# Performance work log

Measured on AMD Instinct MI355X. Metric: run time of the kernel, lower is better.

Reference implementation:

```python
import jax, jax.numpy as jnp
import numpy as np

B, S, D, C, H, E, K, L = 32, 512, 768, 3072, 1024, 8, 2, 2


def _layernorm(x, g, b, eps=1e-5):
    mu = jnp.mean(x, axis=-1, keepdims=True)
    var = jnp.var(x, axis=-1, keepdims=True)
    return (x - mu) * jax.lax.rsqrt(var + eps) * g + b


def setup_inputs() -> dict:
    key = jax.random.key(0)
    ks = jax.random.split(key, 12)
    s = 0.02
    return {
        "hidden_states": jax.random.normal(ks[0], (B, S, C), jnp.float32),
        "proj_w": jax.random.normal(ks[1], (C, D), jnp.float32) * s,
        "proj_b": jnp.zeros((D,), jnp.float32),
        "ln1_g": jnp.ones((D,), jnp.float32),
        "ln1_b": jnp.zeros((D,), jnp.float32),
        "gate_w": jax.random.normal(ks[2], (D, E), jnp.float32) * s,
        "gate_b": jnp.zeros((E,), jnp.float32),
        "w1": jax.random.normal(ks[3], (E, D, H), jnp.float32) * s,
        "b1": jnp.zeros((E, H), jnp.float32),
        "w2": jax.random.normal(ks[4], (E, H, D), jnp.float32) * s,
        "b2": jnp.zeros((E, D), jnp.float32),
        "ln2_g": jnp.ones((D,), jnp.float32),
        "ln2_b": jnp.zeros((D,), jnp.float32),
        "cls_w": jax.random.normal(ks[5], (D, L), jnp.float32) * s,
        "cls_b": jnp.zeros((L,), jnp.float32),
    }


def reference(hidden_states, proj_w, proj_b, ln1_g, ln1_b, gate_w, gate_b,
              w1, b1, w2, b2, ln2_g, ln2_b, cls_w, cls_b):
    # layer_projection: Linear -> LayerNorm -> GELU (dropout = identity in eval)
    x = jnp.einsum('bsc,cd->bsd', hidden_states, proj_w) + proj_b
    x = _layernorm(x, ln1_g, ln1_b)
    seq_out = jax.nn.gelu(x, approximate=False)  # [B,S,D]

    # Router: gate -> softmax -> top-k -> renormalize
    probs = jax.nn.softmax(seq_out @ gate_w + gate_b, axis=-1)  # [B,S,E]
    top_w, top_i = jax.lax.top_k(probs, K)                      # [B,S,K]
    top_w = top_w / jnp.sum(top_w, axis=-1, keepdims=True)

    # combine[t,e] = sum_k top_w[t,k] * (top_i[t,k]==e)
    combine = jnp.sum(jax.nn.one_hot(top_i, E, dtype=top_w.dtype)
                      * top_w[..., None], axis=-2)              # [B,S,E]

    xt = seq_out.reshape(-1, D)                                 # [T,D]
    ct = combine.reshape(-1, E)                                 # [T,E]
    h = jax.nn.gelu(jnp.einsum('td,edh->eth', xt, w1) + b1[:, None, :],
                    approximate=False)                          # [E,T,H]
    eo = jnp.einsum('eth,ehd->etd', h, w2) + b2[:, None, :]     # [E,T,D]
    moe = jnp.einsum('etd,te->td', eo, ct).reshape(B, S, D)

    moe = _layernorm(moe + seq_out, ln2_g, ln2_b)
    logits = moe @ cls_w + cls_b                                # [B,S,2]
    return logits
```

## Files before the change

kernel.cpp:

```cpp
#include <hip/hip_runtime.h>
#include <hip/hip_bf16.h>

#define T_TOK 16384
#define CDIM 3072
#define DDIM 768
#define HDIM 1024
#define NEXP 8
#define NSLOT 33792
#define MAXTILE 264
#define AMB_CAP 2048
#define AMB2_CAP 256
#define KSPLIT 4
#define NSEG 8

typedef __attribute__((ext_vector_type(8))) short bfrag;
typedef __attribute__((ext_vector_type(4))) float f32x4;
typedef __attribute__((ext_vector_type(4))) float fvec4;

__device__ __forceinline__ unsigned short bf16_rn(float f) {
  union { float f; unsigned u; } v; v.f = f;
  unsigned r = v.u + 0x7fffu + ((v.u >> 16) & 1u);
  return (unsigned short)(r >> 16);
}
__device__ __forceinline__ float bf16_f32(unsigned short h) {
  union { unsigned u; float f; } v; v.u = ((unsigned)h) << 16;
  return v.f;
}
__device__ __forceinline__ float gelu_exact(float x) {
  return 0.5f * x * (1.0f + erff(x * 0.70710678118654752440f));
}
__device__ __forceinline__ void glds16(const void* g, void* l) {
  __builtin_amdgcn_global_load_lds((const __attribute__((address_space(1))) void*)g,
                                   (__attribute__((address_space(3))) void*)l, 16, 0, 0);
}

__global__ void k_init(int* token_list, int* counts, int* cursors, unsigned short* zero_row,
                       int* amb_count, int* amb2_count) {
  int i = blockIdx.x * 256 + threadIdx.x;
  for (int j = i; j < NSLOT; j += 64 * 256) token_list[j] = -1;
  if (i < NEXP) counts[i] = 0;
  if (i < 128) cursors[i] = 0;
  if (i == 0) { *amb_count = 0; *amb2_count = 0; }
  if (i < 1024) zero_row[i] = 0;
}

__global__ void k_cast_tiled(const float* __restrict__ src,
                             unsigned short* __restrict__ dst) {
  __shared__ unsigned short h[128][136];
  int rb = blockIdx.x;
  int cc = blockIdx.y;
  int tid = threadIdx.x;
  const float* in = src + ((size_t)rb * 128) * CDIM + cc * 128;
#pragma unroll
  for (int it = 0; it < 16; ++it) {
    int idx = it * 256 + tid;
    int r = idx >> 5, nv = idx & 31;
    fvec4 v = *(const fvec4*)(in + (size_t)r * CDIM + nv * 4);
    unsigned long long p = (unsigned long long)bf16_rn(v[0]) |
                           ((unsigned long long)bf16_rn(v[1]) << 16) |
                           ((unsigned long long)bf16_rn(v[2]) << 32) |
                           ((unsigned long long)bf16_rn(v[3]) << 48);
    *(unsigned long long*)&h[r][nv * 4] = p;
  }
  __syncthreads();
  unsigned short* ob = dst + ((size_t)rb * 96 + cc * 4) * 4096;
#pragma unroll
  for (int kt = 0; kt < 4; ++kt) {
#pragma unroll
    for (int it = 0; it < 2; ++it) {
      int gg = it * 256 + tid;
      int kg = gg >> 7, r = gg & 127;
      bfrag o = *(const bfrag*)&h[r][kt * 32 + kg * 8];
      *(bfrag*)(ob + ((size_t)kt * 512 + gg) * 8) = o;
    }
  }
}

__global__ void k_transpose_split(const float* __restrict__ src,
                                  unsigned short* __restrict__ dhi,
                                  unsigned short* __restrict__ dlo) {
  __shared__ unsigned short h[128][72], l[128][72];
  int nb2 = blockIdx.x;
  int cb = blockIdx.y;
  int col_blk = nb2 >> 1, nhalf = nb2 & 1;
  int n0 = col_blk * 128 + nhalf * 64;
  int tid = threadIdx.x;
  const float* in = src + (size_t)(cb * 128) * DDIM + n0;
#pragma unroll
  for (int it = 0; it < 8; ++it) {
    int idx = it * 256 + tid;
    int cl = idx >> 4, nv = idx & 15;
    fvec4 v = *(const fvec4*)(in + (size_t)cl * DDIM + nv * 4);
    unsigned long long ph = 0, pl = 0;
#pragma unroll
    for (int e = 0; e < 4; ++e) {
      unsigned short hh = bf16_rn(v[e]);
      unsigned short ll = bf16_rn(v[e] - bf16_f32(hh));
      ph |= (unsigned long long)hh << (16 * e);
      pl |= (unsigned long long)ll << (16 * e);
    }
    *(unsigned long long*)&h[cl][nv * 4] = ph;
    *(unsigned long long*)&l[cl][nv * 4] = pl;
  }
  __syncthreads();
  size_t obase = ((size_t)col_blk * 96 + cb * 4) * 4096;
#pragma unroll
  for (int kt = 0; kt < 4; ++kt) {
    int kg = tid >> 6, rl = tid & 63;
    bfrag oh, ol;
#pragma unroll
    for (int e = 0; e < 8; ++e) {
      int c = kt * 32 + kg * 8 + e;
      oh[e] = (short)h[c][rl];
      ol[e] = (short)l[c][rl];
    }
    size_t gi = obase + ((size_t)kt * 512 + kg * 128 + nhalf * 64 + rl) * 8;
    *(bfrag*)(dhi + gi) = oh;
    *(bfrag*)(dlo + gi) = ol;
  }
}

__global__ void k_transpose_tiled(const float* __restrict__ src0,
                                  unsigned short* __restrict__ dst0, int K, int N) {
  __shared__ unsigned short h[128][72];
  int nb2 = blockIdx.x;
  int cb = blockIdx.y;
  int z = blockIdx.z;
  int col_blk = nb2 >> 1, nhalf = nb2 & 1;
  int n0 = col_blk * 128 + nhalf * 64;
  int tid = threadIdx.x;
  const float* in = src0 + (size_t)z * K * N + (size_t)(cb * 128) * N + n0;
#pragma unroll
  for (int it = 0; it < 8; ++it) {
    int idx = it * 256 + tid;
    int cl = idx >> 4, nv = idx & 15;
    fvec4 v = *(const fvec4*)(in + (size_t)cl * N + nv * 4);
    unsigned long long ph = 0;
#pragma unroll
    for (int e = 0; e < 4; ++e)
      ph |= (unsigned long long)bf16_rn(v[e]) << (16 * e);
    *(unsigned long long*)&h[cl][nv * 4] = ph;
  }
  __syncthreads();
  size_t obase = (size_t)z * K * N + ((size_t)col_blk * (K / 32) + cb * 4) * 4096;
#pragma unroll
  for (int kt = 0; kt < 4; ++kt) {
    int kg = tid >> 6, rl = tid & 63;
    bfrag oh;
#pragma unroll
    for (int e = 0; e < 8; ++e) oh[e] = (short)h[kt * 32 + kg * 8 + e][rl];
    *(bfrag*)(dst0 + obase + ((size_t)kt * 512 + kg * 128 + nhalf * 64 + rl) * 8) = oh;
  }
}

__launch_bounds__(256, 3)
__global__ void k_gemm1(const unsigned short* __restrict__ Atil,
                        const unsigned short* __restrict__ Btil,
                        float* __restrict__ Cout)
{
  __shared__ unsigned short sA[12288], sB[12288];
  int tid = threadIdx.x;
  int lane = tid & 63, wave = tid >> 6;
  int id = blockIdx.x;
  int swz = (id & 7) * 96 + (id >> 3);
  int brow = swz / 6, bcol = swz % 6;
  int row0 = brow * 128, col0 = bcol * 128;
  int wm = wave >> 1, wn = wave & 1;

  f32x4 acc[4][4];
#pragma unroll
  for (int i = 0; i < 4; ++i)
#pragma unroll
    for (int j = 0; j < 4; ++j) acc[i][j] = (f32x4){0.f, 0.f, 0.f, 0.f};

  int rsel = lane & 15, kq = lane >> 4;
  const unsigned short* At = Atil + (size_t)(brow * 96) * 4096;
  const unsigned short* Bt = Btil + (size_t)(bcol * 96) * 4096;

  auto STAGE = [&](int kt, int b) {
    const unsigned short* as = At + (size_t)kt * 4096;
    const unsigned short* bs = Bt + (size_t)kt * 4096;
    int lbase = b * 4096;
#pragma unroll
    for (int pass = 0; pass < 2; ++pass) {
      int g = pass * 256 + tid;
      int li = lbase + (pass * 256 + wave * 64) * 8;
      glds16(as + (size_t)g * 8, &sA[li]);
      glds16(bs + (size_t)g * 8, &sB[li]);
    }
  };

  STAGE(0, 0);
  STAGE(1, 1);
  int b0 = 0;
  for (int kt = 0; kt < 96; ++kt) {
    if (kt < 95) asm volatile("s_waitcnt vmcnt(4)" ::: "memory");
    else         asm volatile("s_waitcnt vmcnt(0)" ::: "memory");
    __builtin_amdgcn_s_barrier();
    if (kt + 2 < 96) {
      int bn = b0 + 2; if (bn >= 3) bn -= 3;
      STAGE(kt + 2, bn);
    }
    int lb = b0 * 4096;
    bfrag af[4], bf[4];
#pragma unroll
    for (int i = 0; i < 4; ++i) {
      af[i] = *(const bfrag*)&sA[lb + (kq * 128 + wm * 64 + i * 16 + rsel) * 8];
      bf[i] = *(const bfrag*)&sB[lb + (kq * 128 + wn * 64 + i * 16 + rsel) * 8];
    }
#pragma unroll
    for (int i = 0; i < 4; ++i)
#pragma unroll
      for (int j = 0; j < 4; ++j)
        acc[i][j] = __builtin_amdgcn_mfma_f32_16x16x32_bf16(af[i], bf[j], acc[i][j], 0, 0, 0);
    b0 = (b0 == 2) ? 0 : b0 + 1;
  }

  int cc = lane & 15, rr = (lane >> 4) * 4;
#pragma unroll
  for (int i = 0; i < 4; ++i)
#pragma unroll
    for (int j = 0; j < 4; ++j)
#pragma unroll
      for (int r = 0; r < 4; ++r) {
        int row = row0 + wm * 64 + i * 16 + rr + r;
        int col = col0 + wn * 64 + j * 16 + cc;
        Cout[(size_t)row * DDIM + col] = acc[i][j][r];
      }
}

__launch_bounds__(256)
__global__ void k_ln_router(const float* __restrict__ xw, const float* __restrict__ proj_b,
                            const float* __restrict__ g1, const float* __restrict__ b1v,
                            const float* __restrict__ gate_w, const float* __restrict__ gate_b,
                            unsigned short* __restrict__ seq_b16,
                            int* __restrict__ top_i, float* __restrict__ top_w,
                            int* __restrict__ amb_list, int* __restrict__ amb_count)
{
  int lane = threadIdx.x & 63;
  int t = blockIdx.x * 4 + (threadIdx.x >> 6);
  const float* xr = xw + (size_t)t * DDIM;
  float x0[12];
  float s = 0.f, s2 = 0.f;
#pragma unroll
  for (int j = 0; j < 12; ++j) {
    int d = lane + 64 * j;
    float v = xr[d] + proj_b[d];
    x0[j] = v; s += v; s2 += v * v;
  }
#pragma unroll
  for (int o = 32; o > 0; o >>= 1) { s += __shfl_xor(s, o, 64); s2 += __shfl_xor(s2, o, 64); }
  float mu = s * (1.f / DDIM);
  float rstd = rsqrtf(s2 * (1.f / DDIM) - mu * mu + 1e-5f);
  float acc8[8];
#pragma unroll
  for (int e = 0; e < 8; ++e) acc8[e] = 0.f;
#pragma unroll
  for (int j = 0; j < 12; ++j) {
    int d = lane + 64 * j;
    float y = (x0[j] - mu) * rstd * g1[d] + b1v[d];
    float ge = gelu_exact(y);
    seq_b16[(size_t)t * DDIM + d] = bf16_rn(ge);
    const float* gw = gate_w + (size_t)d * NEXP;
#pragma unroll
    for (int e = 0; e < 8; ++e) acc8[e] += ge * gw[e];
  }
#pragma unroll
  for (int e = 0; e < 8; ++e)
#pragma unroll
    for (int o = 32; o > 0; o >>= 1) acc8[e] += __shfl_xor(acc8[e], o, 64);
  if (lane == 0) {
    float lg[8];
#pragma unroll
    for (int e = 0; e < 8; ++e) lg[e] = acc8[e] + gate_b[e];
    int i0 = 0;
    for (int e = 1; e < 8; ++e) if (lg[e] > lg[i0]) i0 = e;
    int i1 = (i0 == 0) ? 1 : 0;
    for (int e = 0; e < 8; ++e) if (e != i0 && lg[e] > lg[i1]) i1 = e;
    float l2 = -1e30f;
    for (int e = 0; e < 8; ++e) if (e != i0 && e != i1 && lg[e] > l2) l2 = lg[e];
    if (lg[i1] - l2 < 8e-3f) {
      int p = atomicAdd(amb_count, 1);
      if (p < AMB_CAP) amb_list[p] = t;
    }
    float w0 = 1.f / (1.f + expf(lg[i1] - lg[i0]));
    top_i[t * 2] = i0; top_i[t * 2 + 1] = i1;
    top_w[t * 2] = w0; top_w[t * 2 + 1] = 1.f - w0;
  }
}

__launch_bounds__(256, 2)
__global__ void k_repair(const float* __restrict__ hidden,
                         const unsigned short* __restrict__ BTh,
                         const unsigned short* __restrict__ BTl,
                         const int* __restrict__ amb_list, const int* __restrict__ amb_count,
                         float* __restrict__ xw_fix4)
{
  int n = *amb_count; if (n > AMB_CAP) n = AMB_CAP;
  int by = blockIdx.y;
  if (by * 128 >= n) return;
  int bx = blockIdx.x;
  int z = blockIdx.z;
  int col0 = bx * 128;
  __shared__ unsigned short sAh[8192], sAl[8192], sBh[8192], sBl[8192];
  __shared__ int tk[128];
  int tid = threadIdx.x, lane = tid & 63, wave = tid >> 6;
  if (tid < 128) tk[tid] = (by * 128 + tid < n) ? amb_list[by * 128 + tid] : -1;
  __syncthreads();
  int wm = wave >> 1, wn = wave & 1;
  f32x4 acc[4][4];
#pragma unroll
  for (int i = 0; i < 4; ++i)
#pragma unroll
    for (int j = 0; j < 4; ++j) acc[i][j] = (f32x4){0.f, 0.f, 0.f, 0.f};
  int rsel = lane & 15, kq = lane >> 4;
  int ktbase = z * 24;
  const unsigned short* Bth = BTh + (size_t)(bx * 96) * 4096;
  const unsigned short* Btl = BTl + (size_t)(bx * 96) * 4096;

  auto STAGE = [&](int kt, int b) {
    int k0 = (ktbase + kt) * 32;
    int lb = b * 4096;
    size_t tb = (size_t)(ktbase + kt) * 4096;
#pragma unroll
    for (int pass = 0; pass < 2; ++pass) {
      int g = pass * 256 + tid;
      int kg = g >> 7, r = g & 127;
      int tok = tk[r];
      fvec4 a0 = (fvec4){0.f, 0.f, 0.f, 0.f}, a1 = a0;
      if (tok >= 0) {
        const float* ap = hidden + (size_t)tok * CDIM + k0 + kg * 8;
        a0 = *(const fvec4*)ap;
        a1 = *(const fvec4*)(ap + 4);
      }
      bfrag hv, lv;
#pragma unroll
      for (int u = 0; u < 8; ++u) {
        float v = (u < 4) ? a0[u] : a1[u - 4];
        unsigned short h = bf16_rn(v);
        hv[u] = (short)h;
        lv[u] = (short)bf16_rn(v - bf16_f32(h));
      }
      *(bfrag*)&sAh[lb + (size_t)g * 8] = hv;
      *(bfrag*)&sAl[lb + (size_t)g * 8] = lv;
      int li = lb + (pass * 256 + wave * 64) * 8;
      glds16(Bth + tb + (size_t)g * 8, &sBh[li]);
      glds16(Btl + tb + (size_t)g * 8, &sBl[li]);
    }
  };

  STAGE(0, 0);
  __syncthreads();
  for (int kt = 0; kt < 24; ++kt) {
    int b = kt & 1;
    if (kt + 1 < 24) STAGE(kt + 1, b ^ 1);
    int lb = b * 4096;
    bfrag ah[4], al[4], bh[4], bl[4];
#pragma unroll
    for (int i = 0; i < 4; ++i) {
      int ra = wm * 64 + i * 16 + rsel;
      ah[i] = *(const bfrag*)&sAh[lb + (kq * 128 + ra) * 8];
      al[i] = *(const bfrag*)&sAl[lb + (kq * 128 + ra) * 8];
      int cb = wn * 64 + i * 16 + rsel;
      bh[i] = *(const bfrag*)&sBh[lb + (kq * 128 + cb) * 8];
      bl[i] = *(const bfrag*)&sBl[lb + (kq * 128 + cb) * 8];
    }
#pragma unroll
    for (int i = 0; i < 4; ++i)
#pragma unroll
      for (int j = 0; j < 4; ++j) {
        acc[i][j] = __builtin_amdgcn_mfma_f32_16x16x32_bf16(ah[i], bh[j], acc[i][j], 0, 0, 0);
        acc[i][j] = __builtin_amdgcn_mfma_f32_16x16x32_bf16(ah[i], bl[j], acc[i][j], 0, 0, 0);
        acc[i][j] = __builtin_amdgcn_mfma_f32_16x16x32_bf16(al[i], bh[j], acc[i][j], 0, 0, 0);
      }
    __syncthreads();
  }
  float* dst = xw_fix4 + (size_t)z * AMB_CAP * DDIM;
  int cc = lane & 15, rr = (lane >> 4) * 4;
#pragma unroll
  for (int i = 0; i < 4; ++i)
#pragma unroll
    for (int j = 0; j < 4; ++j)
#pragma unroll
      for (int r = 0; r < 4; ++r) {
        int row = by * 128 + wm * 64 + i * 16 + rr + r;
        int col = col0 + wn * 64 + j * 16 + cc;
        dst[(size_t)row * DDIM + col] = acc[i][j][r];
      }
}

__launch_bounds__(256)
__global__ void k_fix2(const float* __restrict__ xw_fix4, const float* __restrict__ proj_b,
                       const float* __restrict__ g1, const float* __restrict__ b1v,
                       const float* __restrict__ gate_w, const float* __restrict__ gate_b,
                       const int* __restrict__ amb_list, const int* __restrict__ amb_count,
                       int* __restrict__ top_i, float* __restrict__ top_w,
                       int* __restrict__ amb2_list, int* __restrict__ amb2_count)
{
  int n = *amb_count; if (n > AMB_CAP) n = AMB_CAP;
  int lane = threadIdx.x & 63;
  int slot = blockIdx.x * 4 + (threadIdx.x >> 6);
  if (slot >= n) return;
  int t = amb_list[slot];
  const float* p0 = xw_fix4 + (size_t)slot * DDIM;
  const float* p1 = p0 + (size_t)AMB_CAP * DDIM;
  const float* p2 = p1 + (size_t)AMB_CAP * DDIM;
  const float* p3 = p2 + (size_t)AMB_CAP * DDIM;
  float x0[12];
  float s = 0.f, s2 = 0.f;
#pragma unroll
  for (int j = 0; j < 12; ++j) {
    int d = lane + 64 * j;
    float v = ((p0[d] + p1[d]) + (p2[d] + p3[d])) + proj_b[d];
    x0[j] = v; s += v; s2 += v * v;
  }
#pragma unroll
  for (int o = 32; o > 0; o >>= 1) { s += __shfl_xor(s, o, 64); s2 += __shfl_xor(s2, o, 64); }
  float mu = s * (1.f / DDIM);
  float rstd = rsqrtf(s2 * (1.f / DDIM) - mu * mu + 1e-5f);
  float acc8[8];
#pragma unroll
  for (int e = 0; e < 8; ++e) acc8[e] = 0.f;
#pragma unroll
  for (int j = 0; j < 12; ++j) {
    int d = lane + 64 * j;
    float y = (x0[j] - mu) * rstd * g1[d] + b1v[d];
    float ge = gelu_exact(y);
    const float* gw = gate_w + (size_t)d * NEXP;
#pragma unroll
    for (int e = 0; e < 8; ++e) acc8[e] += ge * gw[e];
  }
#pragma unroll
  for (int e = 0; e < 8; ++e)
#pragma unroll
    for (int o = 32; o > 0; o >>= 1) acc8[e] += __shfl_xor(acc8[e], o, 64);
  if (lane == 0) {
    float lg[8];
#pragma unroll
    for (int e = 0; e < 8; ++e) lg[e] = acc8[e] + gate_b[e];
    int i0 = 0;
    for (int e = 1; e < 8; ++e) if (lg[e] > lg[i0]) i0 = e;
    int i1 = (i0 == 0) ? 1 : 0;
    for (int e = 0; e < 8; ++e) if (e != i0 && lg[e] > lg[i1]) i1 = e;
    float l2 = -1e30f;
    for (int e = 0; e < 8; ++e) if (e != i0 && e != i1 && lg[e] > l2) l2 = lg[e];
    if (lg[i1] - l2 < 2e-4f) {
      int p = atomicAdd(amb2_count, 1);
      if (p < AMB2_CAP) amb2_list[p] = t;
    }
    float w0 = 1.f / (1.f + expf(lg[i1] - lg[i0]));
    top_i[t * 2] = i0; top_i[t * 2 + 1] = i1;
    top_w[t * 2] = w0; top_w[t * 2 + 1] = 1.f - w0;
  }
}

__launch_bounds__(256, 1)
__global__ void k_router_fix(const float* __restrict__ hidden, const float* __restrict__ proj_w,
                             const int* __restrict__ amb2_list, const int* __restrict__ amb2_count,
                             double* __restrict__ xpart)
{
  __shared__ float hrow[384];
  int tid = threadIdx.x;
  int seg = blockIdx.y;
  int cbase = seg * 384;
  int n = *amb2_count; if (n > AMB2_CAP) n = AMB2_CAP;
  for (int ii = blockIdx.x; ii < n; ii += gridDim.x) {
    int t = amb2_list[ii];
    __syncthreads();
    if (tid < 96)
      *(fvec4*)&hrow[tid * 4] = *(const fvec4*)(hidden + (size_t)t * CDIM + cbase + tid * 4);
    __syncthreads();
    double p0a = 0.0, p0b = 0.0, p1a = 0.0, p1b = 0.0, p2a = 0.0, p2b = 0.0;
    for (int c0 = 0; c0 < 384; c0 += 16) {
      float w0r[16], w1r[16], w2r[16];
      const float* wp = proj_w + (size_t)(cbase + c0) * DDIM + tid;
#pragma unroll
      for (int u = 0; u < 16; ++u) {
        w0r[u] = wp[u * DDIM];
        w1r[u] = wp[u * DDIM + 256];
        w2r[u] = wp[u * DDIM + 512];
      }
#pragma unroll
      for (int u = 0; u < 16; ++u) {
        double h = (double)hrow[c0 + u];
        if (u & 1) { p0b += h * (double)w0r[u]; p1b += h * (double)w1r[u]; p2b += h * (double)w2r[u]; }
        else       { p0a += h * (double)w0r[u]; p1a += h * (double)w1r[u]; p2a += h * (double)w2r[u]; }
      }
    }
    double* xp = xpart + ((size_t)seg * AMB2_CAP + ii) * DDIM;
    xp[tid] = p0a + p0b;
    xp[tid + 256] = p1a + p1b;
    xp[tid + 512] = p2a + p2b;
  }
}

__launch_bounds__(256)
__global__ void k_fix3(const double* __restrict__ xpart, const float* __restrict__ proj_b,
                       const float* __restrict__ g1, const float* __restrict__ b1v,
                       const float* __restrict__ gate_w, const float* __restrict__ gate_b,
                       const int* __restrict__ amb2_list, const int* __restrict__ amb2_count,
                       int* __restrict__ top_i, float* __restrict__ top_w)
{
  __shared__ double redA[4], redB[4], red8[4][8];
  int n = *amb2_count; if (n > AMB2_CAP) n = AMB2_CAP;
  int ii = blockIdx.x;
  if (ii >= n) return;
  int t = amb2_list[ii];
  int tid = threadIdx.x, lane = tid & 63, wave = tid >> 6;
  double x[3]; double s = 0.0, s2 = 0.0;
#pragma unroll
  for (int j = 0; j < 3; ++j) {
    int d = tid + 256 * j;
    double acc = (double)proj_b[d];
#pragma unroll
    for (int seg = 0; seg < NSEG; ++seg)
      acc += xpart[((size_t)seg * AMB2_CAP + ii) * DDIM + d];
    x[j] = acc; s += acc; s2 += acc * acc;
  }
#pragma unroll
  for (int o = 32; o > 0; o >>= 1) { s += __shfl_down(s, o, 64); s2 += __shfl_down(s2, o, 64); }
  if (lane == 0) { redA[wave] = s; redB[wave] = s2; }
  __syncthreads();
  double mu = (redA[0] + redA[1] + redA[2] + redA[3]) / DDIM;
  double ms = (redB[0] + redB[1] + redB[2] + redB[3]) / DDIM;
  double rstd = 1.0 / sqrt(ms - mu * mu + 1e-5);
  double a8[8];
#pragma unroll
  for (int e = 0; e < 8; ++e) a8[e] = 0.0;
#pragma unroll
  for (int j = 0; j < 3; ++j) {
    int d = tid + 256 * j;
    double y = (x[j] - mu) * rstd * (double)g1[d] + (double)b1v[d];
    double ge = 0.5 * y * (1.0 + erf(y * 0.7071067811865475244));
#pragma unroll
    for (int e = 0; e < 8; ++e) a8[e] += ge * (double)gate_w[(size_t)d * NEXP + e];
  }
#pragma unroll
  for (int e = 0; e < 8; ++e)
#pragma unroll
    for (int o = 32; o > 0; o >>= 1) a8[e] += __shfl_down(a8[e], o, 64);
  if (lane == 0) {
#pragma unroll
    for (int e = 0; e < 8; ++e) red8[wave][e] = a8[e];
  }
  __syncthreads();
  if (tid == 0) {
    double lg[8];
#pragma unroll
    for (int e = 0; e < 8; ++e)
      lg[e] = red8[0][e] + red8[1][e] + red8[2][e] + red8[3][e] + (double)gate_b[e];
    int i0 = 0;
    for (int e = 1; e < 8; ++e) if (lg[e] > lg[i0]) i0 = e;
    int i1 = (i0 == 0) ? 1 : 0;
    for (int e = 0; e < 8; ++e) if (e != i0 && e != i1 && lg[e] > lg[i1]) i1 = e;
    double w0 = 1.0 / (1.0 + exp(lg[i1] - lg[i0]));
    top_i[t * 2] = i0; top_i[t * 2 + 1] = i1;
    top_w[t * 2] = (float)w0; top_w[t * 2 + 1] = (float)(1.0 - w0);
  }
}

__global__ void k_count(const int* __restrict__ top_i, int* __restrict__ counts) {
  __shared__ int h[NEXP];
  int tid = threadIdx.x;
  if (tid < NEXP) h[tid] = 0;
  __syncthreads();
  for (int i = blockIdx.x * 256 + tid; i < 2 * T_TOK; i += 64 * 256)
    atomicAdd(&h[top_i[i]], 1);
  __syncthreads();
  if (tid < NEXP) atomicAdd(&counts[tid], h[tid]);
}

__global__ void k_offsets(const int* __restrict__ counts, int* __restrict__ seg_start,
                          int* __restrict__ padded_total, int* __restrict__ tile_expert) {
  if (threadIdx.x != 0 || blockIdx.x != 0) return;
  int st[NEXP], en[NEXP];
  int s = 0;
  for (int e = 0; e < NEXP; ++e) {
    st[e] = s; seg_start[e] = s;
    s += (counts[e] + 127) & ~127;
    en[e] = s;
  }
  *padded_total = s;
  int nt = s >> 7;
  for (int x = 0; x < nt; ++x) {
    int r = x << 7, e = 0;
    for (int q = 0; q < NEXP; ++q) if (r >= st[q] && r < en[q]) e = q;
    tile_expert[x] = e;
  }
}

__global__ void k_scatter(const int* __restrict__ top_i, const int* __restrict__ seg_start,
                          int* __restrict__ cursors, int* __restrict__ token_list,
                          int* __restrict__ slot_of) {
  __shared__ int lc[NEXP];
  __shared__ int lbase[NEXP];
  int tid = threadIdx.x;
  int t = blockIdx.x * 256 + tid;
  if (tid < NEXP) lc[tid] = 0;
  __syncthreads();
  int e0 = top_i[t * 2], e1 = top_i[t * 2 + 1];
  int o0 = atomicAdd(&lc[e0], 1);
  int o1 = atomicAdd(&lc[e1], 1);
  __syncthreads();
  if (tid < NEXP) lbase[tid] = atomicAdd(&cursors[tid << 4], lc[tid]);
  __syncthreads();
  int p0 = seg_start[e0] + lbase[e0] + o0;
  int p1 = seg_start[e1] + lbase[e1] + o1;
  token_list[p0] = t;
  token_list[p1] = t;
  slot_of[t * 2] = p0;
  slot_of[t * 2 + 1] = p1;
}

__global__ void k_gather(const unsigned short* __restrict__ seqb,
                         const int* __restrict__ token_list,
                         const int* __restrict__ padded_total,
                         unsigned short* __restrict__ seqgT) {
  int sb = blockIdx.x;
  if (sb * 128 >= *padded_total) return;
  int cc = blockIdx.y;
  __shared__ unsigned short h[128][136];
  __shared__ int tk[128];
  int tid = threadIdx.x;
  if (tid < 128) tk[tid] = token_list[sb * 128 + tid];
  __syncthreads();
#pragma unroll
  for (int it = 0; it < 8; ++it) {
    int idx = it * 256 + tid;
    int r = idx >> 4, nv = idx & 15;
    int tok = tk[r];
    bfrag v = (bfrag){0, 0, 0, 0, 0, 0, 0, 0};
    if (tok >= 0)
      v = *(const bfrag*)(seqb + (size_t)tok * DDIM + cc * 128 + nv * 8);
    *(bfrag*)&h[r][nv * 8] = v;
  }
  __syncthreads();
  unsigned short* ob = seqgT + ((size_t)sb * 24 + cc * 4) * 4096;
#pragma unroll
  for (int kt = 0; kt < 4; ++kt) {
#pragma unroll
    for (int it = 0; it < 2; ++it) {
      int gg = it * 256 + tid;
      int kg = gg >> 7, r = gg & 127;
      bfrag o = *(const bfrag*)&h[r][kt * 32 + kg * 8];
      *(bfrag*)(ob + ((size_t)kt * 512 + gg) * 8) = o;
    }
  }
}

__launch_bounds__(256, 3)
__global__ void k_gemm2(const unsigned short* __restrict__ seqgT,
                        const unsigned short* __restrict__ w1T,
                        const float* __restrict__ b1,
                        const int* __restrict__ tile_expert,
                        const int* __restrict__ padded_total,
                        unsigned short* __restrict__ hbufT)
{
  int oid = blockIdx.x;
  int xcd = oid & 7, w = oid >> 3;
  int by = xcd * 33 + (w >> 3);
  int bx = w & 7;
  if (by * 128 >= *padded_total) return;
  int e = tile_expert[by];
  __shared__ unsigned short smem[24576];
  unsigned short* sA = smem;
  unsigned short* sB = smem + 12288;
  int tid = threadIdx.x, lane = tid & 63, wave = tid >> 6;
  int col0 = bx * 128;
  int wm = wave >> 1, wn = wave & 1;
  f32x4 acc[4][4];
#pragma unroll
  for (int i = 0; i < 4; ++i)
#pragma unroll
    for (int j = 0; j < 4; ++j) acc[i][j] = (f32x4){0.f, 0.f, 0.f, 0.f};
  const unsigned short* At = seqgT + (size_t)by * 24 * 4096;
  const unsigned short* Bt = w1T + (size_t)e * HDIM * DDIM + (size_t)bx * 24 * 4096;
  int rsel = lane & 15, kq = lane >> 4;

  auto STAGE = [&](int kt, int b) {
    int lbase2 = b * 4096;
    size_t tb = (size_t)kt * 4096;
#pragma unroll
    for (int pass = 0; pass < 2; ++pass) {
      int g = pass * 256 + tid;
      int li = lbase2 + (pass * 256 + wave * 64) * 8;
      glds16(At + tb + (size_t)g * 8, &sA[li]);
      glds16(Bt + tb + (size_t)g * 8, &sB[li]);
    }
  };

  STAGE(0, 0);
  STAGE(1, 1);
  int b0 = 0;
  for (int kt = 0; kt < 24; ++kt) {
    if (kt < 23) asm volatile("s_waitcnt vmcnt(4)" ::: "memory");
    else         asm volatile("s_waitcnt vmcnt(0)" ::: "memory");
    __builtin_amdgcn_s_barrier();
    if (kt + 2 < 24) {
      int bn = b0 + 2; if (bn >= 3) bn -= 3;
      STAGE(kt + 2, bn);
    }
    int lb = b0 * 4096;
    bfrag af[4], bf[4];
#pragma unroll
    for (int i = 0; i < 4; ++i) {
      af[i] = *(const bfrag*)&sA[lb + (kq * 128 + wm * 64 + i * 16 + rsel) * 8];
      bf[i] = *(const bfrag*)&sB[lb + (kq * 128 + wn * 64 + i * 16 + rsel) * 8];
    }
#pragma unroll
    for (int i = 0; i < 4; ++i)
#pragma unroll
      for (int j = 0; j < 4; ++j)
        acc[i][j] = __builtin_amdgcn_mfma_f32_16x16x32_bf16(af[i], bf[j], acc[i][j], 0, 0, 0);
    b0 = (b0 == 2) ? 0 : b0 + 1;
  }
  __builtin_amdgcn_s_barrier();
  int cc = lane & 15, rr = (lane >> 4) * 4;
#pragma unroll
  for (int i = 0; i < 4; ++i)
#pragma unroll
    for (int j = 0; j < 4; ++j)
#pragma unroll
      for (int r = 0; r < 4; ++r) {
        int lr = wm * 64 + i * 16 + rr + r;
        int lc = wn * 64 + j * 16 + cc;
        float x = acc[i][j][r] + b1[(size_t)e * HDIM + col0 + lc];
        int gi = (lc >> 5) * 4096 + ((lc >> 3) & 3) * 1024 + lr * 8 + (lc & 7);
        smem[gi] = bf16_rn(gelu_exact(x));
      }
  __syncthreads();
  unsigned short* dst = hbufT + ((size_t)by * 32 + (col0 >> 5)) * 4096;
#pragma unroll
  for (int it = 0; it < 8; ++it) {
    int idx = it * 256 + tid;
    *(bfrag*)(dst + (size_t)idx * 8) = *(const bfrag*)&smem[idx * 8];
  }
}

__launch_bounds__(256, 3)
__global__ void k_gemm3(const unsigned short* __restrict__ hbufT,
                        const unsigned short* __restrict__ w2T,
                        const float* __restrict__ b2,
                        const int* __restrict__ tile_expert,
                        const int* __restrict__ padded_total,
                        unsigned short* __restrict__ eo)
{
  int oid = blockIdx.x;
  int xcd = oid & 7, w = oid >> 3;
  int by = xcd * 33 + (w / 6);
  int bx = w % 6;
  if (by * 128 >= *padded_total) return;
  int e = tile_expert[by];
  __shared__ unsigned short smem[24576];
  unsigned short* sA = smem;
  unsigned short* sB = smem + 12288;
  int tid = threadIdx.x, lane = tid & 63, wave = tid >> 6;
  int col0 = bx * 128;
  int wm = wave >> 1, wn = wave & 1;
  f32x4 acc[4][4];
#pragma unroll
  for (int i = 0; i < 4; ++i)
#pragma unroll
    for (int j = 0; j < 4; ++j) acc[i][j] = (f32x4){0.f, 0.f, 0.f, 0.f};
  const unsigned short* At = hbufT + (size_t)by * 32 * 4096;
  const unsigned short* Bt = w2T + (size_t)e * DDIM * HDIM + (size_t)bx * 32 * 4096;
  int rsel = lane & 15, kq = lane >> 4;

  auto STAGE = [&](int kt, int b) {
    int lbase2 = b * 4096;
    size_t tb = (size_t)kt * 4096;
#pragma unroll
    for (int pass = 0; pass < 2; ++pass) {
      int g = pass * 256 + tid;
      int li = lbase2 + (pass * 256 + wave * 64) * 8;
      glds16(At + tb + (size_t)g * 8, &sA[li]);
      glds16(Bt + tb + (size_t)g * 8, &sB[li]);
    }
  };

  STAGE(0, 0);
  STAGE(1, 1);
  int b0 = 0;
  for (int kt = 0; kt < 32; ++kt) {
    if (kt < 31) asm volatile("s_waitcnt vmcnt(4)" ::: "memory");
    else         asm volatile("s_waitcnt vmcnt(0)" ::: "memory");
    __builtin_amdgcn_s_barrier();
    if (kt + 2 < 32) {
      int bn = b0 + 2; if (bn >= 3) bn -= 3;
      STAGE(kt + 2, bn);
    }
    int lb = b0 * 4096;
    bfrag af[4], bf[4];
#pragma unroll
    for (int i = 0; i < 4; ++i) {
      af[i] = *(const bfrag*)&sA[lb + (kq * 128 + wm * 64 + i * 16 + rsel) * 8];
      bf[i] = *(const bfrag*)&sB[lb + (kq * 128 + wn * 64 + i * 16 + rsel) * 8];
    }
#pragma unroll
    for (int i = 0; i < 4; ++i)
#pragma unroll
      for (int j = 0; j < 4; ++j)
        acc[i][j] = __builtin_amdgcn_mfma_f32_16x16x32_bf16(af[i], bf[j], acc[i][j], 0, 0, 0);
    b0 = (b0 == 2) ? 0 : b0 + 1;
  }
  __builtin_amdgcn_s_barrier();
  int cc = lane & 15, rr = (lane >> 4) * 4;
#pragma unroll
  for (int i = 0; i < 4; ++i)
#pragma unroll
    for (int j = 0; j < 4; ++j)
#pragma unroll
      for (int r = 0; r < 4; ++r) {
        int lr = wm * 64 + i * 16 + rr + r;
        int lc = wn * 64 + j * 16 + cc;
        smem[lr * 128 + lc] = bf16_rn(acc[i][j][r] + b2[(size_t)e * DDIM + col0 + lc]);
      }
  __syncthreads();
#pragma unroll
  for (int it = 0; it < 8; ++it) {
    int idx = it * 256 + tid;
    int row = idx >> 4, cb = idx & 15;
    *(bfrag*)(eo + (size_t)(by * 128 + row) * DDIM + col0 + cb * 8) =
        *(const bfrag*)&smem[row * 128 + cb * 8];
  }
}

__launch_bounds__(256)
__global__ void k_combine(const unsigned short* __restrict__ eo,
                          const unsigned short* __restrict__ seqb,
                          const int* __restrict__ slot_of, const float* __restrict__ top_w,
                          const float* __restrict__ g2, const float* __restrict__ b2v,
                          const float* __restrict__ cls_w, const float* __restrict__ cls_b,
                          float* __restrict__ out)
{
  int lane = threadIdx.x & 63;
  int t = blockIdx.x * 4 + (threadIdx.x >> 6);
  int s0 = slot_of[t * 2], s1 = slot_of[t * 2 + 1];
  float w0 = top_w[t * 2], w1 = top_w[t * 2 + 1];
  const unsigned short* p0 = eo + (size_t)s0 * DDIM;
  const unsigned short* p1 = eo + (size_t)s1 * DDIM;
  const unsigned short* sq = seqb + (size_t)t * DDIM;
  float m[12];
  float s = 0.f, s2 = 0.f;
#pragma unroll
  for (int j = 0; j < 12; ++j) {
    int d = lane + 64 * j;
    float v = w0 * bf16_f32(p0[d]) + w1 * bf16_f32(p1[d]) + bf16_f32(sq[d]);
    m[j] = v; s += v; s2 += v * v;
  }
#pragma unroll
  for (int o = 32; o > 0; o >>= 1) { s += __shfl_xor(s, o, 64); s2 += __shfl_xor(s2, o, 64); }
  float mu = s * (1.f / DDIM);
  float rstd = rsqrtf(s2 * (1.f / DDIM) - mu * mu + 1e-5f);
  float l0 = 0.f, l1 = 0.f;
#pragma unroll
  for (int j = 0; j < 12; ++j) {
    int d = lane + 64 * j;
    float y = (m[j] - mu) * rstd * g2[d] + b2v[d];
    l0 += y * cls_w[d * 2];
    l1 += y * cls_w[d * 2 + 1];
  }
#pragma unroll
  for (int o = 32; o > 0; o >>= 1) { l0 += __shfl_xor(l0, o, 64); l1 += __shfl_xor(l1, o, 64); }
  if (lane == 0) {
    out[(size_t)t * 2] = l0 + cls_b[0];
    out[(size_t)t * 2 + 1] = l1 + cls_b[1];
  }
}

extern "C" void kernel_launch(void* const* d_in, const int* in_sizes, int n_in,
                              void* d_out, int out_size, void* d_ws, size_t ws_size,
                              hipStream_t stream) {
  const float* hidden = (const float*)d_in[0];
  const float* proj_w = (const float*)d_in[1];
  const float* proj_b = (const float*)d_in[2];
  const float* ln1_g  = (const float*)d_in[3];
  const float* ln1_b  = (const float*)d_in[4];
  const float* gate_w = (const float*)d_in[5];
  const float* gate_b = (const float*)d_in[6];
  const float* w1     = (const float*)d_in[7];
  const float* b1     = (const float*)d_in[8];
  const float* w2     = (const float*)d_in[9];
  const float* b2     = (const float*)d_in[10];
  const float* ln2_g  = (const float*)d_in[11];
  const float* ln2_b  = (const float*)d_in[12];
  const float* cls_w  = (const float*)d_in[13];
  const float* cls_b  = (const float*)d_in[14];
  float* out = (float*)d_out;

  char* base = (char*)d_ws;
  size_t off = 0;
  auto alloc = [&](size_t b) -> void* {
    void* p = base + off;
    off += (b + 255) & ~(size_t)255;
    return p;
  };
  unsigned short* pwT_hi = (unsigned short*)alloc((size_t)DDIM * CDIM * 2);
  unsigned short* pwT_lo = (unsigned short*)alloc((size_t)DDIM * CDIM * 2);
  unsigned short* w1T    = (unsigned short*)alloc((size_t)NEXP * HDIM * DDIM * 2);
  unsigned short* w2T    = (unsigned short*)alloc((size_t)NEXP * DDIM * HDIM * 2);
  float* xw              = (float*)alloc((size_t)T_TOK * DDIM * 4);
  float* xw_fix4         = (float*)alloc((size_t)KSPLIT * AMB_CAP * DDIM * 4);
  double* xpart          = (double*)alloc((size_t)NSEG * AMB2_CAP * DDIM * 8);
  unsigned short* seqb   = (unsigned short*)alloc((size_t)T_TOK * DDIM * 2);
  unsigned short* seqgT  = (unsigned short*)alloc((size_t)MAXTILE * 24 * 4096 * 2);
  int* top_i             = (int*)alloc((size_t)T_TOK * 2 * 4);
  float* top_w           = (float*)alloc((size_t)T_TOK * 2 * 4);
  int* slot_of           = (int*)alloc((size_t)T_TOK * 2 * 4);
  int* amb_list          = (int*)alloc((size_t)AMB_CAP * 4);
  int* amb2_list         = (int*)alloc((size_t)AMB2_CAP * 4);
  int* token_list        = (int*)alloc((size_t)NSLOT * 4);
  int* counts            = (int*)alloc(256);
  int* cursors           = (int*)alloc(512);
  int* seg_start         = (int*)alloc(256);
  int* padded_total      = (int*)alloc(256);
  int* tile_expert       = (int*)alloc((size_t)MAXTILE * 4);
  unsigned short* zero_row = (unsigned short*)alloc(2048);
  int* amb_count         = (int*)alloc(256);
  int* amb2_count        = (int*)alloc(256);
  size_t poolBytes = 2 * (size_t)T_TOK * CDIM * 2;
  char* pool = (char*)alloc(poolBytes);
  unsigned short* Ahi = (unsigned short*)pool;
  size_t poff = 0;
  auto palloc = [&](size_t b) -> void* {
    void* p = pool + poff;
    poff += (b + 255) & ~(size_t)255;
    return p;
  };
  unsigned short* hbufT  = (unsigned short*)palloc((size_t)MAXTILE * 32 * 4096 * 2);
  unsigned short* eo     = (unsigned short*)palloc((size_t)NSLOT * DDIM * 2);
  (void)ws_size; (void)in_sizes; (void)n_in; (void)out_size;

  k_init<<<64, 256, 0, stream>>>(token_list, counts, cursors, zero_row, amb_count, amb2_count);
  k_cast_tiled<<<dim3(128, 24), 256, 0, stream>>>(hidden, Ahi);
  k_transpose_split<<<dim3(12, 24), 256, 0, stream>>>(proj_w, pwT_hi, pwT_lo);
  k_transpose_tiled<<<dim3(16, 6, 8), 256, 0, stream>>>(w1, w1T, DDIM, HDIM);
  k_transpose_tiled<<<dim3(12, 8, 8), 256, 0, stream>>>(w2, w2T, HDIM, DDIM);
  k_gemm1<<<768, 256, 0, stream>>>(Ahi, pwT_hi, xw);
  k_ln_router<<<T_TOK / 4, 256, 0, stream>>>(xw, proj_b, ln1_g, ln1_b, gate_w, gate_b,
                                             seqb, top_i, top_w, amb_list, amb_count);
  k_repair<<<dim3(6, AMB_CAP / 128, KSPLIT), 256, 0, stream>>>(hidden, pwT_hi, pwT_lo,
                                                               amb_list, amb_count, xw_fix4);
  k_fix2<<<AMB_CAP / 4, 256, 0, stream>>>(xw_fix4, proj_b, ln1_g, ln1_b, gate_w, gate_b,
                                          amb_list, amb_count, top_i, top_w,
                                          amb2_list, amb2_count);
  k_router_fix<<<dim3(64, NSEG), 256, 0, stream>>>(hidden, proj_w, amb2_list, amb2_count, xpart);
  k_fix3<<<AMB2_CAP, 256, 0, stream>>>(xpart, proj_b, ln1_g, ln1_b, gate_w, gate_b,
                                       amb2_list, amb2_count, top_i, top_w);
  k_count<<<64, 256, 0, stream>>>(top_i, counts);
  k_offsets<<<1, 64, 0, stream>>>(counts, seg_start, padded_total, tile_expert);
  k_scatter<<<64, 256, 0, stream>>>(top_i, seg_start, cursors, token_list, slot_of);
  k_gather<<<dim3(MAXTILE, 6), 256, 0, stream>>>(seqb, token_list, padded_total, seqgT);
  k_gemm2<<<MAXTILE * 8, 256, 0, stream>>>(seqgT, w1T, b1, tile_expert,
                                           padded_total, hbufT);
  k_gemm3<<<MAXTILE * 6, 256, 0, stream>>>(hbufT, w2T, b2, tile_expert, padded_total, eo);
  k_combine<<<T_TOK / 4, 256, 0, stream>>>(eo, seqb, slot_of, top_w, ln2_g, ln2_b,
                                           cls_w, cls_b, out);
}
```

Measured before the change: 573.4 us.

## Fuse token gather into expert GEMM A-operand loads

Removes the separate gather kernel that copied routed token rows into a tiled buffer. The first expert GEMM now loads its A operand directly from the dense activation rows via the token list, and padded slots read from a zero row. This drops one kernel launch and a full write and read of the gathered buffer. In exchange, the A loads become per-row scattered 16-byte reads, each row is re-read by all 8 column-tile blocks, and the loads may coalesce less well.

```diff
diff --git a/kernel.cpp b/kernel.cpp
--- a/kernel.cpp
+++ b/kernel.cpp
@@ -612,46 +612,12 @@
   slot_of[t * 2 + 1] = p1;
 }
 
-__global__ void k_gather(const unsigned short* __restrict__ seqb,
-                         const int* __restrict__ token_list,
-                         const int* __restrict__ padded_total,
-                         unsigned short* __restrict__ seqgT) {
-  int sb = blockIdx.x;
-  if (sb * 128 >= *padded_total) return;
-  int cc = blockIdx.y;
-  __shared__ unsigned short h[128][136];
-  __shared__ int tk[128];
-  int tid = threadIdx.x;
-  if (tid < 128) tk[tid] = token_list[sb * 128 + tid];
-  __syncthreads();
-#pragma unroll
-  for (int it = 0; it < 8; ++it) {
-    int idx = it * 256 + tid;
-    int r = idx >> 4, nv = idx & 15;
-    int tok = tk[r];
-    bfrag v = (bfrag){0, 0, 0, 0, 0, 0, 0, 0};
-    if (tok >= 0)
-      v = *(const bfrag*)(seqb + (size_t)tok * DDIM + cc * 128 + nv * 8);
-    *(bfrag*)&h[r][nv * 8] = v;
-  }
-  __syncthreads();
-  unsigned short* ob = seqgT + ((size_t)sb * 24 + cc * 4) * 4096;
-#pragma unroll
-  for (int kt = 0; kt < 4; ++kt) {
-#pragma unroll
-    for (int it = 0; it < 2; ++it) {
-      int gg = it * 256 + tid;
-      int kg = gg >> 7, r = gg & 127;
-      bfrag o = *(const bfrag*)&h[r][kt * 32 + kg * 8];
-      *(bfrag*)(ob + ((size_t)kt * 512 + gg) * 8) = o;
-    }
-  }
-}
-
 __launch_bounds__(256, 3)
-__global__ void k_gemm2(const unsigned short* __restrict__ seqgT,
+__global__ void k_gemm2(const unsigned short* __restrict__ seqb,
                         const unsigned short* __restrict__ w1T,
                         const float* __restrict__ b1,
+                        const int* __restrict__ token_list,
+                        const unsigned short* __restrict__ zero_row,
                         const int* __restrict__ tile_expert,
                         const int* __restrict__ padded_total,
                         unsigned short* __restrict__ hbufT)
@@ -673,20 +639,29 @@
   for (int i = 0; i < 4; ++i)
 #pragma unroll
     for (int j = 0; j < 4; ++j) acc[i][j] = (f32x4){0.f, 0.f, 0.f, 0.f};
-  const unsigned short* At = seqgT + (size_t)by * 24 * 4096;
+  int tokreg = token_list[by * 128 + (tid & 127)];
+  const unsigned short* a0;
+  const unsigned short* a1;
+  int astep;
+  if (tokreg >= 0) {
+    a0 = seqb + (size_t)tokreg * DDIM + (tid >> 7) * 8;
+    a1 = a0 + 16;
+    astep = 32;
+  } else {
+    a0 = zero_row + (tid >> 7) * 8;
+    a1 = a0 + 16;
+    astep = 0;
+  }
   const unsigned short* Bt = w1T + (size_t)e * HDIM * DDIM + (size_t)bx * 24 * 4096;
   int rsel = lane & 15, kq = lane >> 4;
 
   auto STAGE = [&](int kt, int b) {
     int lbase2 = b * 4096;
     size_t tb = (size_t)kt * 4096;
-#pragma unroll
-    for (int pass = 0; pass < 2; ++pass) {
-      int g = pass * 256 + tid;
-      int li = lbase2 + (pass * 256 + wave * 64) * 8;
-      glds16(At + tb + (size_t)g * 8, &sA[li]);
-      glds16(Bt + tb + (size_t)g * 8, &sB[li]);
-    }
+    glds16(a0 + (size_t)kt * astep, &sA[lbase2 + (wave * 64) * 8]);
+    glds16(Bt + tb + (size_t)tid * 8, &sB[lbase2 + (wave * 64) * 8]);
+    glds16(a1 + (size_t)kt * astep, &sA[lbase2 + (256 + wave * 64) * 8]);
+    glds16(Bt + tb + (size_t)(256 + tid) * 8, &sB[lbase2 + (256 + wave * 64) * 8]);
   };
 
   STAGE(0, 0);
@@ -903,7 +878,6 @@
   float* xw_fix4         = (float*)alloc((size_t)KSPLIT * AMB_CAP * DDIM * 4);
   double* xpart          = (double*)alloc((size_t)NSEG * AMB2_CAP * DDIM * 8);
   unsigned short* seqb   = (unsigned short*)alloc((size_t)T_TOK * DDIM * 2);
-  unsigned short* seqgT  = (unsigned short*)alloc((size_t)MAXTILE * 24 * 4096 * 2);
   int* top_i             = (int*)alloc((size_t)T_TOK * 2 * 4);
   float* top_w           = (float*)alloc((size_t)T_TOK * 2 * 4);
   int* slot_of           = (int*)alloc((size_t)T_TOK * 2 * 4);
@@ -950,9 +924,8 @@
   k_count<<<64, 256, 0, stream>>>(top_i, counts);
   k_offsets<<<1, 64, 0, stream>>>(counts, seg_start, padded_total, tile_expert);
   k_scatter<<<64, 256, 0, stream>>>(top_i, seg_start, cursors, token_list, slot_of);
-  k_gather<<<dim3(MAXTILE, 6), 256, 0, stream>>>(seqb, token_list, padded_total, seqgT);
-  k_gemm2<<<MAXTILE * 8, 256, 0, stream>>>(seqgT, w1T, b1, tile_expert,
-                                           padded_total, hbufT);
+  k_gemm2<<<MAXTILE * 8, 256, 0, stream>>>(seqb, w1T, b1, token_list, zero_row,
+                                           tile_expert, padded_total, hbufT);
   k_gemm3<<<MAXTILE * 6, 256, 0, stream>>>(hbufT, w2T, b2, tile_expert, padded_total, eo);
   k_combine<<<T_TOK / 4, 256, 0, stream>>>(eo, seqb, slot_of, top_w, ln2_g, ln2_b,
                                            cls_w, cls_b, out);
```

After: 556.0 us (median of 3 runs). -3.0%, faster.
